# Optimization experiments

Measured on AMD Instinct MI355X. Metric: run time of the kernel, lower is better.

## Reference

```python
import jax, jax.numpy as jnp
import numpy as np

B, T, D_IN, H, NL = 4096, 512, 32, 16, 2


def setup_inputs() -> dict:
    key = jax.random.key(0)
    ks = jax.random.split(key, 16)
    s = lambda fan: 1.0 / np.sqrt(H)  # PyTorch LSTM init scale: U(-1/sqrt(H), 1/sqrt(H))
    u = lambda k, shape: jax.random.uniform(k, shape, jnp.float32, -s(H), s(H))
    inp = {
        "x": jax.random.normal(ks[0], (B, T, D_IN), jnp.float32),
        # layer 0 (gate order i, f, g, o as in PyTorch)
        "Wih0": u(ks[1], (4 * H, D_IN)),
        "Whh0": u(ks[2], (4 * H, H)),
        "bih0": u(ks[3], (4 * H,)),
        "bhh0": u(ks[4], (4 * H,)),
        # layer 1
        "Wih1": u(ks[5], (4 * H, H)),
        "Whh1": u(ks[6], (4 * H, H)),
        "bih1": u(ks[7], (4 * H,)),
        "bhh1": u(ks[8], (4 * H,)),
        # MLP head
        "fc1_w": u(ks[9], (8, H)),
        "fc1_b": u(ks[10], (8,)),
        "fc2_w": u(ks[11], (1, 8)),
        "fc2_b": u(ks[12], (1,)),
    }
    return inp


def _lstm_layer(x_seq, Wih, Whh, bih, bhh):
    # x_seq: [B, T, D]; returns all hidden states [B, T, H]
    b = bih + bhh
    # precompute input projections for all timesteps: [T, B, 4H]
    xg = jnp.einsum("btd,gd->tbg", x_seq, Wih) + b
    h0 = jnp.zeros((x_seq.shape[0], H), x_seq.dtype)
    c0 = jnp.zeros_like(h0)

    def step(carry, xt):
        h, c = carry
        gates = xt + h @ Whh.T  # [B, 4H]
        i, f, g, o = jnp.split(gates, 4, axis=-1)
        i, f, o = jax.nn.sigmoid(i), jax.nn.sigmoid(f), jax.nn.sigmoid(o)
        g = jnp.tanh(g)
        c = f * c + i * g
        h = o * jnp.tanh(c)
        return (h, c), h

    _, hs = jax.lax.scan(step, (h0, c0), xg)  # hs: [T, B, H]
    return jnp.transpose(hs, (1, 0, 2))


def reference(x, Wih0, Whh0, bih0, bhh0, Wih1, Whh1, bih1, bhh1, fc1_w, fc1_b, fc2_w, fc2_b):
    h1 = _lstm_layer(x, Wih0, Whh0, bih0, bhh0)   # [B, T, H]
    h2 = _lstm_layer(h1, Wih1, Whh1, bih1, bhh1)  # [B, T, H]
    last = h2[:, -1, :]                            # [B, H]
    y = jax.nn.relu(last @ fc1_w.T + fc1_b)        # [B, 8]
    return y @ fc2_w.T + fc2_b                     # [B, 1]
```

## Files before the change

### kernel.cpp

```cpp
#include <hip/hip_runtime.h>
#include <stdint.h>

#define T_STEPS 512
#define D_INP   32
#define CHUNK   8
#define NCHUNK  (T_STEPS / CHUNK)

typedef float f2 __attribute__((ext_vector_type(2)));
typedef float f4 __attribute__((ext_vector_type(4)));

typedef const uint32_t __attribute__((address_space(1)))* gas1_t;
typedef uint32_t __attribute__((address_space(3)))* las3_t;

#define LOG2E 1.44269504088896f
#define TANHK (-2.88539008177793f)

template <int K>
__device__ __forceinline__ float qbcast(float v) {
  return __int_as_float(
      __builtin_amdgcn_mov_dpp(__float_as_int(v), K * 85, 0xF, 0xF, true));
}

__device__ __forceinline__ float frcp(float v) { return __builtin_amdgcn_rcpf(v); }
__device__ __forceinline__ float fexp2(float v) { return __builtin_amdgcn_exp2f(v); }
__device__ __forceinline__ f2 lo2(f4 v) { return __builtin_shufflevector(v, v, 0, 1); }
__device__ __forceinline__ f2 hi2(f4 v) { return __builtin_shufflevector(v, v, 2, 3); }
__device__ __forceinline__ f2 pkfma(f2 a, f2 b, f2 c) {
  return __builtin_elementwise_fma(a, b, c);
}

extern "C" __global__ void __launch_bounds__(256)
lstm2_fused(const float* __restrict__ x,
            const float* __restrict__ Wih0, const float* __restrict__ Whh0,
            const float* __restrict__ bih0, const float* __restrict__ bhh0,
            const float* __restrict__ Wih1, const float* __restrict__ Whh1,
            const float* __restrict__ bih1, const float* __restrict__ bhh1,
            const float* __restrict__ fc1w, const float* __restrict__ fc1b,
            const float* __restrict__ fc2w, const float* __restrict__ fc2b,
            float* __restrict__ out)
{
  __shared__ __align__(16) float lx[4][2][CHUNK * D_INP];
  __shared__ __align__(16) float lh0[4][80];
  __shared__ __align__(16) float lh1[4][80];

  const int tid  = threadIdx.x;
  const int w    = tid >> 6;
  const int lane = tid & 63;
  const int b    = (blockIdx.x << 2) + w;

  const int k   = lane & 3;
  const int u   = lane >> 2;
  const int row = k * 16 + u;

  const float sc = (k == 2) ? -2.0f * LOG2E : -LOG2E;
  const float mA = (k == 2) ?  2.0f : 1.0f;
  const float aA = (k == 2) ? -1.0f : 0.0f;

  f2 wi0[16], wh0[8], wi1[8], wh1[8];
  {
    const f4* p = (const f4*)(Wih0 + row * 32);
#pragma unroll
    for (int q = 0; q < 8; ++q) {
      f4 v = p[q];
      wi0[2 * q + 0] = lo2(v) * sc;
      wi0[2 * q + 1] = hi2(v) * sc;
    }
    const f4* p0 = (const f4*)(Whh0 + row * 16);
    const f4* p1 = (const f4*)(Wih1 + row * 16);
    const f4* p2 = (const f4*)(Whh1 + row * 16);
#pragma unroll
    for (int q = 0; q < 4; ++q) {
      f4 a = p0[q], bq = p1[q], cq = p2[q];
      wh0[2 * q] = lo2(a) * sc;  wh0[2 * q + 1] = hi2(a) * sc;
      wi1[2 * q] = lo2(bq) * sc; wi1[2 * q + 1] = hi2(bq) * sc;
      wh1[2 * q] = lo2(cq) * sc; wh1[2 * q + 1] = hi2(cq) * sc;
    }
  }
  const float bs0 = sc * (bih0[row] + bhh0[row]);
  const float bs1 = sc * (bih1[row] + bhh1[row]);

  const int slot = (k == 0) ? u : (16 + lane);
  float* h0slot = &lh0[w][slot];
  float* h1slot = &lh1[w][slot];

  float c0 = 0.f, c1 = 0.f;
  f2 h0p[8];
#pragma unroll
  for (int j = 0; j < 8; ++j) h0p[j] = (f2){0.f, 0.f};
  if (lane < 16) lh1[w][lane] = 0.f;

  const float* xg = x + (size_t)b * (T_STEPS * D_INP);

  {
    const float* src = xg + lane * 4;
    __builtin_amdgcn_global_load_lds((gas1_t)(const void*)src,
                                     (las3_t)(void*)&lx[w][0][0], 16, 0, 0);
  }

#pragma unroll 1
  for (int c = 0; c < NCHUNK; ++c) {
    asm volatile("s_waitcnt vmcnt(0)" ::: "memory");
    if (c + 1 < NCHUNK) {
      const float* src = xg + (c + 1) * (CHUNK * D_INP) + lane * 4;
      __builtin_amdgcn_global_load_lds((gas1_t)(const void*)src,
                                       (las3_t)(void*)&lx[w][(c + 1) & 1][0],
                                       16, 0, 0);
    }
    const float* xp = &lx[w][c & 1][0];
#pragma unroll
    for (int tt = 0; tt < CHUNK; ++tt) {
      const float* xq = xp + tt * D_INP;
      f4 hA = *(const f4*)(&lh1[w][0]);
      f4 hB = *(const f4*)(&lh1[w][4]);
      f4 hC = *(const f4*)(&lh1[w][8]);
      f4 hD = *(const f4*)(&lh1[w][12]);
      f2 b01 = (f2){bs1, 0.f}, b23 = (f2){0.f, 0.f};
      b01 = pkfma(wh1[0], lo2(hA), b01);  b23 = pkfma(wh1[1], hi2(hA), b23);
      b01 = pkfma(wh1[2], lo2(hB), b01);  b23 = pkfma(wh1[3], hi2(hB), b23);
      b01 = pkfma(wh1[4], lo2(hC), b01);  b23 = pkfma(wh1[5], hi2(hC), b23);
      b01 = pkfma(wh1[6], lo2(hD), b01);  b23 = pkfma(wh1[7], hi2(hD), b23);
      f2 a01 = (f2){bs0, 0.f}, a23 = (f2){0.f, 0.f};
#pragma unroll
      for (int q = 0; q < 8; ++q) {
        f4 v = *(const f4*)(xq + 4 * q);
        a01 = pkfma(wi0[2 * q + 0], lo2(v), a01);
        a23 = pkfma(wi0[2 * q + 1], hi2(v), a23);
      }
#pragma unroll
      for (int q = 0; q < 4; ++q) {
        a01 = pkfma(wh0[2 * q + 0], h0p[2 * q + 0], a01);
        a23 = pkfma(wh0[2 * q + 1], h0p[2 * q + 1], a23);
      }
      f2 asum = a01 + a23;
      float gs = asum.x + asum.y;
      float av = fmaf(mA, frcp(1.f + fexp2(gs)), aA);
      float fv = qbcast<1>(av), gv = qbcast<2>(av), ov = qbcast<3>(av);
      c0 = fmaf(fv, c0, av * gv);
      float th = fmaf(2.f, frcp(1.f + fexp2(TANHK * c0)), -1.f);
      float h0n = ov * th;
      *h0slot = h0n;
#pragma unroll
      for (int q = 0; q < 4; ++q) {
        f4 hv = *(const f4*)(&lh0[w][4 * q]);
        h0p[2 * q + 0] = lo2(hv);
        h0p[2 * q + 1] = hi2(hv);
      }
#pragma unroll
      for (int q = 0; q < 4; ++q) {
        b01 = pkfma(wi1[2 * q + 0], h0p[2 * q + 0], b01);
        b23 = pkfma(wi1[2 * q + 1], h0p[2 * q + 1], b23);
      }
      f2 bsum = b01 + b23;
      float gs1 = bsum.x + bsum.y;
      float av1 = fmaf(mA, frcp(1.f + fexp2(gs1)), aA);
      float fv1 = qbcast<1>(av1), gv1 = qbcast<2>(av1), ov1 = qbcast<3>(av1);
      c1 = fmaf(fv1, c1, av1 * gv1);
      float th1 = fmaf(2.f, frcp(1.f + fexp2(TANHK * c1)), -1.f);
      float h1n = ov1 * th1;
      *h1slot = h1n;
    }
  }

  float h1f[16];
#pragma unroll
  for (int q = 0; q < 4; ++q) {
    f4 hv = *(const f4*)(&lh1[w][4 * q]);
#pragma unroll
    for (int r = 0; r < 4; ++r) h1f[4 * q + r] = hv[r];
  }
  float rr = 0.f;
  if (lane < 8) {
    float acc = fc1b[lane];
#pragma unroll
    for (int j = 0; j < 16; ++j) acc = fmaf(fc1w[lane * 16 + j], h1f[j], acc);
    rr = fmaxf(acc, 0.f) * fc2w[lane];
  }
  rr += __shfl_xor(rr, 1, 64);
  rr += __shfl_xor(rr, 2, 64);
  rr += __shfl_xor(rr, 4, 64);
  if (lane == 0) out[b] = rr + fc2b[0];
}

extern "C" void kernel_launch(void* const* d_in, const int* in_sizes, int n_in,
                              void* d_out, int out_size, void* d_ws, size_t ws_size,
                              hipStream_t stream) {
  (void)in_sizes; (void)n_in; (void)d_ws; (void)ws_size; (void)out_size;
  const float* x    = (const float*)d_in[0];
  const float* Wih0 = (const float*)d_in[1];
  const float* Whh0 = (const float*)d_in[2];
  const float* bih0 = (const float*)d_in[3];
  const float* bhh0 = (const float*)d_in[4];
  const float* Wih1 = (const float*)d_in[5];
  const float* Whh1 = (const float*)d_in[6];
  const float* bih1 = (const float*)d_in[7];
  const float* bhh1 = (const float*)d_in[8];
  const float* fc1w = (const float*)d_in[9];
  const float* fc1b = (const float*)d_in[10];
  const float* fc2w = (const float*)d_in[11];
  const float* fc2b = (const float*)d_in[12];
  lstm2_fused<<<dim3(1024), dim3(256), 0, stream>>>(
      x, Wih0, Whh0, bih0, bhh0, Wih1, Whh1, bih1, bhh1,
      fc1w, fc1b, fc2w, fc2b, (float*)d_out);
}
```

Measured before the change: 408.7 us.

## Precompute next chunk's layer-0 input projections ahead of the recurrent steps

The layer-0 input projection (Wih0·x_t plus bias) is moved out of the per-step recurrent chain. It is now computed for a whole chunk one chunk ahead, into a register array, while the recurrence for the current chunk uses the values already computed. The x prefetch is pushed two chunks ahead to match, and the loop is unrolled by two so the ping-pong register arrays stay statically indexed. This shortens the serial dependency chain of each timestep. It costs 16 extra registers for the projection buffers and some wasted projection work on the final chunk.

Result: slower. 693.6 us (+69.7%).

```diff
diff --git a/kernel.cpp b/kernel.cpp
--- a/kernel.cpp
+++ b/kernel.cpp
@@ -20,7 +20,6 @@
   return __int_as_float(
       __builtin_amdgcn_mov_dpp(__float_as_int(v), K * 85, 0xF, 0xF, true));
 }
-
 __device__ __forceinline__ float frcp(float v) { return __builtin_amdgcn_rcpf(v); }
 __device__ __forceinline__ float fexp2(float v) { return __builtin_amdgcn_exp2f(v); }
 __device__ __forceinline__ f2 lo2(f4 v) { return __builtin_shufflevector(v, v, 0, 1); }
@@ -30,14 +29,14 @@
 }
 
 extern "C" __global__ void __launch_bounds__(256)
-lstm2_fused(const float* __restrict__ x,
-            const float* __restrict__ Wih0, const float* __restrict__ Whh0,
-            const float* __restrict__ bih0, const float* __restrict__ bhh0,
-            const float* __restrict__ Wih1, const float* __restrict__ Whh1,
-            const float* __restrict__ bih1, const float* __restrict__ bhh1,
-            const float* __restrict__ fc1w, const float* __restrict__ fc1b,
-            const float* __restrict__ fc2w, const float* __restrict__ fc2b,
-            float* __restrict__ out)
+lstm2_xg(const float* __restrict__ x,
+         const float* __restrict__ Wih0, const float* __restrict__ Whh0,
+         const float* __restrict__ bih0, const float* __restrict__ bhh0,
+         const float* __restrict__ Wih1, const float* __restrict__ Whh1,
+         const float* __restrict__ bih1, const float* __restrict__ bhh1,
+         const float* __restrict__ fc1w, const float* __restrict__ fc1b,
+         const float* __restrict__ fc2w, const float* __restrict__ fc2b,
+         float* __restrict__ out)
 {
   __shared__ __align__(16) float lx[4][2][CHUNK * D_INP];
   __shared__ __align__(16) float lh0[4][80];
@@ -89,27 +88,59 @@
   for (int j = 0; j < 8; ++j) h0p[j] = (f2){0.f, 0.f};
   if (lane < 16) lh1[w][lane] = 0.f;
 
-  const float* xg = x + (size_t)b * (T_STEPS * D_INP);
+  const float* xgp = x + (size_t)b * (T_STEPS * D_INP);
 
   {
-    const float* src = xg + lane * 4;
+    const float* src = xgp + lane * 4;
     __builtin_amdgcn_global_load_lds((gas1_t)(const void*)src,
                                      (las3_t)(void*)&lx[w][0][0], 16, 0, 0);
   }
-
-#pragma unroll 1
-  for (int c = 0; c < NCHUNK; ++c) {
+  asm volatile("s_waitcnt vmcnt(0)" ::: "memory");
+  {
+    const float* src = xgp + (CHUNK * D_INP) + lane * 4;
+    __builtin_amdgcn_global_load_lds((gas1_t)(const void*)src,
+                                     (las3_t)(void*)&lx[w][1][0], 16, 0, 0);
+  }
+
+  float xgA[CHUNK], xgB[CHUNK];
+#pragma unroll
+  for (int tt = 0; tt < CHUNK; ++tt) {
+    const float* xq = &lx[w][0][tt * D_INP];
+    f2 g01 = (f2){bs0, 0.f}, g23 = (f2){0.f, 0.f};
+#pragma unroll
+    for (int q = 0; q < 8; ++q) {
+      f4 v = *(const f4*)(xq + 4 * q);
+      g01 = pkfma(wi0[2 * q + 0], lo2(v), g01);
+      g23 = pkfma(wi0[2 * q + 1], hi2(v), g23);
+    }
+    f2 gsum = g01 + g23;
+    xgA[tt] = gsum.x + gsum.y;
+  }
+
+  auto chunk_body = [&](int c, float (&xgc)[CHUNK], float (&xgn)[CHUNK]) {
     asm volatile("s_waitcnt vmcnt(0)" ::: "memory");
-    if (c + 1 < NCHUNK) {
-      const float* src = xg + (c + 1) * (CHUNK * D_INP) + lane * 4;
+    if (c + 2 < NCHUNK) {
+      const float* src = xgp + (c + 2) * (CHUNK * D_INP) + lane * 4;
       __builtin_amdgcn_global_load_lds((gas1_t)(const void*)src,
-                                       (las3_t)(void*)&lx[w][(c + 1) & 1][0],
+                                       (las3_t)(void*)&lx[w][c & 1][0],
                                        16, 0, 0);
     }
-    const float* xp = &lx[w][c & 1][0];
+    const float* xp = &lx[w][(c + 1) & 1][0];
 #pragma unroll
     for (int tt = 0; tt < CHUNK; ++tt) {
       const float* xq = xp + tt * D_INP;
+      f2 g01 = (f2){bs0, 0.f}, g23 = (f2){0.f, 0.f};
+#pragma unroll
+      for (int q = 0; q < 8; ++q) {
+        f4 v = *(const f4*)(xq + 4 * q);
+        g01 = pkfma(wi0[2 * q + 0], lo2(v), g01);
+        g23 = pkfma(wi0[2 * q + 1], hi2(v), g23);
+      }
+      f2 gsum = g01 + g23;
+      xgn[tt] = gsum.x + gsum.y;
+    }
+#pragma unroll
+    for (int tt = 0; tt < CHUNK; ++tt) {
       f4 hA = *(const f4*)(&lh1[w][0]);
       f4 hB = *(const f4*)(&lh1[w][4]);
       f4 hC = *(const f4*)(&lh1[w][8]);
@@ -119,13 +150,7 @@
       b01 = pkfma(wh1[2], lo2(hB), b01);  b23 = pkfma(wh1[3], hi2(hB), b23);
       b01 = pkfma(wh1[4], lo2(hC), b01);  b23 = pkfma(wh1[5], hi2(hC), b23);
       b01 = pkfma(wh1[6], lo2(hD), b01);  b23 = pkfma(wh1[7], hi2(hD), b23);
-      f2 a01 = (f2){bs0, 0.f}, a23 = (f2){0.f, 0.f};
-#pragma unroll
-      for (int q = 0; q < 8; ++q) {
-        f4 v = *(const f4*)(xq + 4 * q);
-        a01 = pkfma(wi0[2 * q + 0], lo2(v), a01);
-        a23 = pkfma(wi0[2 * q + 1], hi2(v), a23);
-      }
+      f2 a01 = (f2){xgc[tt], 0.f}, a23 = (f2){0.f, 0.f};
 #pragma unroll
       for (int q = 0; q < 4; ++q) {
         a01 = pkfma(wh0[2 * q + 0], h0p[2 * q + 0], a01);
@@ -159,6 +184,12 @@
       float h1n = ov1 * th1;
       *h1slot = h1n;
     }
+  };
+
+#pragma unroll 1
+  for (int cc = 0; cc < NCHUNK; cc += 2) {
+    chunk_body(cc,     xgA, xgB);
+    chunk_body(cc + 1, xgB, xgA);
   }
 
   float h1f[16];
@@ -198,7 +229,7 @@
   const float* fc1b = (const float*)d_in[10];
   const float* fc2w = (const float*)d_in[11];
   const float* fc2b = (const float*)d_in[12];
-  lstm2_fused<<<dim3(1024), dim3(256), 0, stream>>>(
+  lstm2_xg<<<dim3(1024), dim3(256), 0, stream>>>(
       x, Wih0, Whh0, bih0, bhh0, Wih1, Whh1, bih1, bhh1,
       fc1w, fc1b, fc2w, fc2b, (float*)d_out);
 }
```

## Split LSTM gate dot products across quad lanes with DPP reduction

Applied to the files above, without the earlier changes.

Instead of each lane computing one full gate row dot product over all inputs, each lane in a quad now computes partial sums for all four gates over a quarter of the input dimension, then reduces across the quad with DPP rotations and selects its own gate. This cuts per-lane FMA count and LDS reads of x/h per step, shortening the serial recurrence latency. It adds DPP reduction steps and selects on the critical path, and changes how weights are held in registers.

Result: slower. 530.2 us (+29.7%).

```diff
diff --git a/kernel.cpp b/kernel.cpp
--- a/kernel.cpp
+++ b/kernel.cpp
@@ -20,7 +20,18 @@
   return __int_as_float(
       __builtin_amdgcn_mov_dpp(__float_as_int(v), K * 85, 0xF, 0xF, true));
 }
-
+template <int CTRL>
+__device__ __forceinline__ f2 qrot(f2 v) {
+  f2 r;
+  r.x = __int_as_float(__builtin_amdgcn_mov_dpp(__float_as_int(v.x), CTRL, 0xF, 0xF, true));
+  r.y = __int_as_float(__builtin_amdgcn_mov_dpp(__float_as_int(v.y), CTRL, 0xF, 0xF, true));
+  return r;
+}
+__device__ __forceinline__ f2 qreduce(f2 v) {
+  v = v + qrot<0x39>(v);
+  v = v + qrot<0x4E>(v);
+  return v;
+}
 __device__ __forceinline__ float frcp(float v) { return __builtin_amdgcn_rcpf(v); }
 __device__ __forceinline__ float fexp2(float v) { return __builtin_amdgcn_exp2f(v); }
 __device__ __forceinline__ f2 lo2(f4 v) { return __builtin_shufflevector(v, v, 0, 1); }
@@ -30,14 +41,14 @@
 }
 
 extern "C" __global__ void __launch_bounds__(256)
-lstm2_fused(const float* __restrict__ x,
-            const float* __restrict__ Wih0, const float* __restrict__ Whh0,
-            const float* __restrict__ bih0, const float* __restrict__ bhh0,
-            const float* __restrict__ Wih1, const float* __restrict__ Whh1,
-            const float* __restrict__ bih1, const float* __restrict__ bhh1,
-            const float* __restrict__ fc1w, const float* __restrict__ fc1b,
-            const float* __restrict__ fc2w, const float* __restrict__ fc2b,
-            float* __restrict__ out)
+lstm2_qs(const float* __restrict__ x,
+         const float* __restrict__ Wih0, const float* __restrict__ Whh0,
+         const float* __restrict__ bih0, const float* __restrict__ bhh0,
+         const float* __restrict__ Wih1, const float* __restrict__ Whh1,
+         const float* __restrict__ bih1, const float* __restrict__ bhh1,
+         const float* __restrict__ fc1w, const float* __restrict__ fc1b,
+         const float* __restrict__ fc2w, const float* __restrict__ fc2b,
+         float* __restrict__ out)
 {
   __shared__ __align__(16) float lx[4][2][CHUNK * D_INP];
   __shared__ __align__(16) float lh0[4][80];
@@ -56,25 +67,22 @@
   const float mA = (k == 2) ?  2.0f : 1.0f;
   const float aA = (k == 2) ? -1.0f : 0.0f;
 
-  f2 wi0[16], wh0[8], wi1[8], wh1[8];
-  {
-    const f4* p = (const f4*)(Wih0 + row * 32);
-#pragma unroll
-    for (int q = 0; q < 8; ++q) {
-      f4 v = p[q];
-      wi0[2 * q + 0] = lo2(v) * sc;
-      wi0[2 * q + 1] = hi2(v) * sc;
-    }
-    const f4* p0 = (const f4*)(Whh0 + row * 16);
-    const f4* p1 = (const f4*)(Wih1 + row * 16);
-    const f4* p2 = (const f4*)(Whh1 + row * 16);
-#pragma unroll
-    for (int q = 0; q < 4; ++q) {
-      f4 a = p0[q], bq = p1[q], cq = p2[q];
-      wh0[2 * q] = lo2(a) * sc;  wh0[2 * q + 1] = hi2(a) * sc;
-      wi1[2 * q] = lo2(bq) * sc; wi1[2 * q + 1] = hi2(bq) * sc;
-      wh1[2 * q] = lo2(cq) * sc; wh1[2 * q + 1] = hi2(cq) * sc;
-    }
+  f2 wx[4][4], wh[4][2], vi[4][2], vh[4][2];
+#pragma unroll
+  for (int g = 0; g < 4; ++g) {
+    const float scg = (g == 2) ? -2.0f * LOG2E : -LOG2E;
+    const int r = g * 16 + u;
+    const float* p0 = Wih0 + r * 32 + 8 * k;
+    f4 va = *(const f4*)(p0);
+    f4 vb = *(const f4*)(p0 + 4);
+    wx[g][0] = lo2(va) * scg; wx[g][1] = hi2(va) * scg;
+    wx[g][2] = lo2(vb) * scg; wx[g][3] = hi2(vb) * scg;
+    f4 vc = *(const f4*)(Whh0 + r * 16 + 4 * k);
+    wh[g][0] = lo2(vc) * scg; wh[g][1] = hi2(vc) * scg;
+    f4 vd = *(const f4*)(Wih1 + r * 16 + 4 * k);
+    vi[g][0] = lo2(vd) * scg; vi[g][1] = hi2(vd) * scg;
+    f4 ve = *(const f4*)(Whh1 + r * 16 + 4 * k);
+    vh[g][0] = lo2(ve) * scg; vh[g][1] = hi2(ve) * scg;
   }
   const float bs0 = sc * (bih0[row] + bhh0[row]);
   const float bs1 = sc * (bih1[row] + bhh1[row]);
@@ -84,9 +92,7 @@
   float* h1slot = &lh1[w][slot];
 
   float c0 = 0.f, c1 = 0.f;
-  f2 h0p[8];
-#pragma unroll
-  for (int j = 0; j < 8; ++j) h0p[j] = (f2){0.f, 0.f};
+  f2 h0a = (f2){0.f, 0.f}, h0b = (f2){0.f, 0.f};
   if (lane < 16) lh1[w][lane] = 0.f;
 
   const float* xg = x + (size_t)b * (T_STEPS * D_INP);
@@ -109,49 +115,50 @@
     const float* xp = &lx[w][c & 1][0];
 #pragma unroll
     for (int tt = 0; tt < CHUNK; ++tt) {
-      const float* xq = xp + tt * D_INP;
-      f4 hA = *(const f4*)(&lh1[w][0]);
-      f4 hB = *(const f4*)(&lh1[w][4]);
-      f4 hC = *(const f4*)(&lh1[w][8]);
-      f4 hD = *(const f4*)(&lh1[w][12]);
-      f2 b01 = (f2){bs1, 0.f}, b23 = (f2){0.f, 0.f};
-      b01 = pkfma(wh1[0], lo2(hA), b01);  b23 = pkfma(wh1[1], hi2(hA), b23);
-      b01 = pkfma(wh1[2], lo2(hB), b01);  b23 = pkfma(wh1[3], hi2(hB), b23);
-      b01 = pkfma(wh1[4], lo2(hC), b01);  b23 = pkfma(wh1[5], hi2(hC), b23);
-      b01 = pkfma(wh1[6], lo2(hD), b01);  b23 = pkfma(wh1[7], hi2(hD), b23);
-      f2 a01 = (f2){bs0, 0.f}, a23 = (f2){0.f, 0.f};
-#pragma unroll
-      for (int q = 0; q < 8; ++q) {
-        f4 v = *(const f4*)(xq + 4 * q);
-        a01 = pkfma(wi0[2 * q + 0], lo2(v), a01);
-        a23 = pkfma(wi0[2 * q + 1], hi2(v), a23);
-      }
-#pragma unroll
-      for (int q = 0; q < 4; ++q) {
-        a01 = pkfma(wh0[2 * q + 0], h0p[2 * q + 0], a01);
-        a23 = pkfma(wh0[2 * q + 1], h0p[2 * q + 1], a23);
-      }
-      f2 asum = a01 + a23;
-      float gs = asum.x + asum.y;
+      const float* xq = xp + tt * D_INP + 8 * k;
+      f4 xa = *(const f4*)(xq);
+      f4 xb = *(const f4*)(xq + 4);
+      f2 x0 = lo2(xa), x1 = hi2(xa), x2 = lo2(xb), x3 = hi2(xb);
+      f4 h1v = *(const f4*)(&lh1[w][4 * k]);
+      f2 e0 = lo2(h1v), e1 = hi2(h1v);
+
+      f2 A0 = wx[0][0] * x0, A1 = wx[1][0] * x0, A2 = wx[2][0] * x0, A3 = wx[3][0] * x0;
+      A0 = pkfma(wx[0][1], x1, A0); A1 = pkfma(wx[1][1], x1, A1);
+      A2 = pkfma(wx[2][1], x1, A2); A3 = pkfma(wx[3][1], x1, A3);
+      A0 = pkfma(wx[0][2], x2, A0); A1 = pkfma(wx[1][2], x2, A1);
+      A2 = pkfma(wx[2][2], x2, A2); A3 = pkfma(wx[3][2], x2, A3);
+      A0 = pkfma(wx[0][3], x3, A0); A1 = pkfma(wx[1][3], x3, A1);
+      A2 = pkfma(wx[2][3], x3, A2); A3 = pkfma(wx[3][3], x3, A3);
+      A0 = pkfma(wh[0][0], h0a, A0); A1 = pkfma(wh[1][0], h0a, A1);
+      A2 = pkfma(wh[2][0], h0a, A2); A3 = pkfma(wh[3][0], h0a, A3);
+      A0 = pkfma(wh[0][1], h0b, A0); A1 = pkfma(wh[1][1], h0b, A1);
+      A2 = pkfma(wh[2][1], h0b, A2); A3 = pkfma(wh[3][1], h0b, A3);
+      A0 = qreduce(A0); A1 = qreduce(A1); A2 = qreduce(A2); A3 = qreduce(A3);
+      f2 t01 = (k & 1) ? A1 : A0;
+      f2 t23 = (k & 1) ? A3 : A2;
+      f2 ownA = (k & 2) ? t23 : t01;
+      float gs = ownA.x + ownA.y + bs0;
       float av = fmaf(mA, frcp(1.f + fexp2(gs)), aA);
       float fv = qbcast<1>(av), gv = qbcast<2>(av), ov = qbcast<3>(av);
       c0 = fmaf(fv, c0, av * gv);
       float th = fmaf(2.f, frcp(1.f + fexp2(TANHK * c0)), -1.f);
       float h0n = ov * th;
       *h0slot = h0n;
-#pragma unroll
-      for (int q = 0; q < 4; ++q) {
-        f4 hv = *(const f4*)(&lh0[w][4 * q]);
-        h0p[2 * q + 0] = lo2(hv);
-        h0p[2 * q + 1] = hi2(hv);
-      }
-#pragma unroll
-      for (int q = 0; q < 4; ++q) {
-        b01 = pkfma(wi1[2 * q + 0], h0p[2 * q + 0], b01);
-        b23 = pkfma(wi1[2 * q + 1], h0p[2 * q + 1], b23);
-      }
-      f2 bsum = b01 + b23;
-      float gs1 = bsum.x + bsum.y;
+      f4 h0v = *(const f4*)(&lh0[w][4 * k]);
+      h0a = lo2(h0v); h0b = hi2(h0v);
+
+      f2 B0 = vi[0][0] * h0a, B1 = vi[1][0] * h0a, B2 = vi[2][0] * h0a, B3 = vi[3][0] * h0a;
+      B0 = pkfma(vi[0][1], h0b, B0); B1 = pkfma(vi[1][1], h0b, B1);
+      B2 = pkfma(vi[2][1], h0b, B2); B3 = pkfma(vi[3][1], h0b, B3);
+      B0 = pkfma(vh[0][0], e0, B0); B1 = pkfma(vh[1][0], e0, B1);
+      B2 = pkfma(vh[2][0], e0, B2); B3 = pkfma(vh[3][0], e0, B3);
+      B0 = pkfma(vh[0][1], e1, B0); B1 = pkfma(vh[1][1], e1, B1);
+      B2 = pkfma(vh[2][1], e1, B2); B3 = pkfma(vh[3][1], e1, B3);
+      B0 = qreduce(B0); B1 = qreduce(B1); B2 = qreduce(B2); B3 = qreduce(B3);
+      f2 s01 = (k & 1) ? B1 : B0;
+      f2 s23 = (k & 1) ? B3 : B2;
+      f2 ownB = (k & 2) ? s23 : s01;
+      float gs1 = ownB.x + ownB.y + bs1;
       float av1 = fmaf(mA, frcp(1.f + fexp2(gs1)), aA);
       float fv1 = qbcast<1>(av1), gv1 = qbcast<2>(av1), ov1 = qbcast<3>(av1);
       c1 = fmaf(fv1, c1, av1 * gv1);
@@ -198,7 +205,7 @@
   const float* fc1b = (const float*)d_in[10];
   const float* fc2w = (const float*)d_in[11];
   const float* fc2b = (const float*)d_in[12];
-  lstm2_fused<<<dim3(1024), dim3(256), 0, stream>>>(
+  lstm2_qs<<<dim3(1024), dim3(256), 0, stream>>>(
       x, Wih0, Whh0, bih0, bhh0, Wih1, Whh1, bih1, bhh1,
       fc1w, fc1b, fc2w, fc2b, (float*)d_out);
 }
```
